# Kernel tuning notes

Hardware: AMD Instinct MI355X
Metric: run time of the kernel (lower is better)

Reference implementation:

```python
import jax, jax.numpy as jnp
import numpy as np

NUM_CLASSES = 4      # config.class_num (malaria stages)
N = 2048             # total nodes = source + target samples
S = 1024             # source_length
FEAT_IN = 25088      # VGG19 include_top=False -> 7*7*512 flattened
D_FC = 512           # Dense(512)
D_G1 = 512           # config.features_dim (GCNConv1 out)
D_G2 = 256           # config.GCN_hidderlayer_dim_num (GCNConv2 out)


def setup_inputs() -> dict:
    key = jax.random.key(0)
    ks = jax.random.split(key, 8)
    sc = lambda fan_in: np.float32(1.0 / np.sqrt(fan_in))
    return {
        "x": jax.random.normal(ks[0], (N, FEAT_IN), jnp.float32),
        "W_fc": jax.random.normal(ks[1], (FEAT_IN, D_FC), jnp.float32) * sc(FEAT_IN),
        "b_fc": jnp.zeros((D_FC,), jnp.float32),
        "W_g1": jax.random.normal(ks[2], (D_FC, D_G1), jnp.float32) * sc(D_FC),
        "b_g1": jnp.zeros((D_G1,), jnp.float32),
        "W_g2": jax.random.normal(ks[3], (D_G1, D_G2), jnp.float32) * sc(D_G1),
        "b_g2": jnp.zeros((D_G2,), jnp.float32),
        "source_labels": jax.random.randint(ks[4], (S,), 0, NUM_CLASSES),
        "source_length": S,
    }


def reference(x, W_fc, b_fc, W_g1, b_g1, W_g2, b_g2, source_labels, source_length):
    # fc after (omitted frozen) VGG19 backbone + flatten
    feats = x @ W_fc + b_fc                                   # [N, 512]

    # get_centers: per-class SUM of source features (no averaging, faithful)
    src = feats[:source_length]                               # [S, 512]
    centers = jax.ops.segment_sum(src, source_labels, num_segments=NUM_CLASSES)  # [C, 512]

    # per-target euclidean distance to each centroid + argmin
    # (argmin of squared distance == argmin of euclidean distance)
    tgt = feats[source_length:]                               # [T, 512]
    d2 = (jnp.sum(tgt * tgt, axis=1, keepdims=True)
          - 2.0 * (tgt @ centers.T)
          + jnp.sum(centers * centers, axis=1)[None, :])      # [T, C]
    target_labels = jnp.argmin(d2, axis=1)                    # [T] int

    # label-cluster graph: edge iff same label; source block forced to identity
    all_labels = jnp.concatenate([source_labels.astype(jnp.int32),
                                  target_labels.astype(jnp.int32)])
    adj = (all_labels[:, None] == all_labels[None, :]).astype(feats.dtype)  # [N, N]
    adj = adj.at[:source_length, :source_length].set(
        jnp.eye(source_length, dtype=feats.dtype))

    # add_self_loops(value=1) then symmetric gcn_filter D^-1/2 A D^-1/2
    A = adj + jnp.eye(N, dtype=feats.dtype)
    dinv = jax.lax.rsqrt(jnp.sum(A, axis=1))                  # [N]
    A_norm = dinv[:, None] * A * dinv[None, :]                # [N, N]

    # two GCN layers (spektral GCNConv: A_norm @ (X @ W) + b) with relu
    h = jax.nn.relu(A_norm @ (feats @ W_g1) + b_g1)           # [N, 512]
    h = jax.nn.relu(A_norm @ (h @ W_g2) + b_g2)               # [N, 256]
    return (h, A_norm, feats)
```

## Files before the change

### kernel.cpp

```cpp
#include <hip/hip_runtime.h>

#define NROWS 2048
#define SLEN  1024
#define FEAT  25088
#define DFC   512
#define DG1   512
#define DG2   256
#define CSPLIT 128

typedef __attribute__((ext_vector_type(8))) short short8;
typedef __attribute__((ext_vector_type(4))) float f32x4;

__device__ __forceinline__ unsigned short bfbits(float f) {
  unsigned int u = __float_as_uint(f);
  u += 0x7fffu + ((u >> 16) & 1u);
  return (unsigned short)(u >> 16);
}

__device__ __forceinline__ unsigned int cvtpk(float lo, float hi) {
  unsigned int r;
  asm("v_cvt_pk_bf16_f32 %0, %1, %2" : "=v"(r) : "v"(lo), "v"(hi));
  return r;
}

__device__ __forceinline__ void load_lds16(const void* g, void* l) {
  __builtin_amdgcn_global_load_lds(
      (const __attribute__((address_space(1))) unsigned int*)g,
      (__attribute__((address_space(3))) unsigned int*)l, 16, 0, 0);
}

__global__ void transpose_cvt_k(const float* __restrict__ src, unsigned short* __restrict__ dst,
                                int K, int Ncol) {
  __shared__ float tile[64][65];
  int kb = blockIdx.x * 64, nb = blockIdx.y * 64;
  int tx = threadIdx.x & 63, ty = threadIdx.x >> 6;
  #pragma unroll
  for (int i = ty; i < 64; i += 4)
    tile[i][tx] = src[(size_t)(kb + i) * Ncol + (nb + tx)];
  __syncthreads();
  #pragma unroll
  for (int i = ty; i < 64; i += 4)
    dst[(size_t)(nb + i) * K + (kb + tx)] = bfbits(tile[tx][i]);
}

__global__ __launch_bounds__(256, 4) void gemm_fc_k(const float* __restrict__ A,
    const unsigned short* __restrict__ BT, float* __restrict__ Cacc, int ksteps) {
  __shared__ unsigned short Al[128 * 32];
  __shared__ unsigned short Bl[128 * 32];
  const int K = FEAT;
  int tid = threadIdx.x;
  int m0 = (blockIdx.x >> 2) * 128;
  int n0 = (blockIdx.x & 3) * 128;
  int kbase = blockIdx.y * ksteps * 32;
  int wid = tid >> 6, lane = tid & 63;
  int wm = wid >> 1, wn = wid & 1;
  int lrow = lane & 15, lko = lane >> 4;

  int chA0 = tid, rA0 = chA0 >> 2, cA0 = chA0 & 3, pA0 = cA0 ^ ((rA0 >> 1) & 3);
  int chA1 = tid + 256, rA1 = chA1 >> 2, cA1 = chA1 & 3, pA1 = cA1 ^ ((rA1 >> 1) & 3);
  int chB0 = wid * 128 + lane;
  int chB1 = wid * 128 + 64 + lane;
  int rB0 = chB0 >> 2, cB0 = (chB0 & 3) ^ ((rB0 >> 1) & 3);
  int rB1 = chB1 >> 2, cB1 = (chB1 & 3) ^ ((rB1 >> 1) & 3);
  const float* gA0 = A + (size_t)(m0 + rA0) * K + cA0 * 8;
  const float* gA1 = A + (size_t)(m0 + rA1) * K + cA1 * 8;
  const unsigned short* gB0 = BT + (size_t)(n0 + rB0) * K + cB0 * 8;
  const unsigned short* gB1 = BT + (size_t)(n0 + rB1) * K + cB1 * 8;

  f32x4 acc[4][4];
  #pragma unroll
  for (int i = 0; i < 4; i++)
    #pragma unroll
    for (int j = 0; j < 4; j++) acc[i][j] = (f32x4){0.f, 0.f, 0.f, 0.f};

  for (int t = 0; t < ksteps; ++t) {
    int k0 = kbase + t * 32;
    float4 v00 = *reinterpret_cast<const float4*>(gA0 + k0);
    float4 v01 = *reinterpret_cast<const float4*>(gA0 + k0 + 4);
    float4 v10 = *reinterpret_cast<const float4*>(gA1 + k0);
    float4 v11 = *reinterpret_cast<const float4*>(gA1 + k0 + 4);
    int4 o0, o1;
    o0.x = (int)cvtpk(v00.x, v00.y); o0.y = (int)cvtpk(v00.z, v00.w);
    o0.z = (int)cvtpk(v01.x, v01.y); o0.w = (int)cvtpk(v01.z, v01.w);
    o1.x = (int)cvtpk(v10.x, v10.y); o1.y = (int)cvtpk(v10.z, v10.w);
    o1.z = (int)cvtpk(v11.x, v11.y); o1.w = (int)cvtpk(v11.z, v11.w);
    __syncthreads();
    *reinterpret_cast<int4*>((char*)Al + rA0 * 64 + pA0 * 16) = o0;
    *reinterpret_cast<int4*>((char*)Al + rA1 * 64 + pA1 * 16) = o1;
    load_lds16(gB0 + k0, (char*)Bl + chB0 * 16);
    load_lds16(gB1 + k0, (char*)Bl + chB1 * 16);
    __syncthreads();
    short8 af[4], bfv[4];
    #pragma unroll
    for (int mi = 0; mi < 4; mi++) {
      int R = wm * 64 + mi * 16 + lrow;
      int p = lko ^ ((R >> 1) & 3);
      af[mi] = *reinterpret_cast<const short8*>((char*)Al + R * 64 + p * 16);
    }
    #pragma unroll
    for (int ni = 0; ni < 4; ni++) {
      int R = wn * 64 + ni * 16 + lrow;
      int p = lko ^ ((R >> 1) & 3);
      bfv[ni] = *reinterpret_cast<const short8*>((char*)Bl + R * 64 + p * 16);
    }
    #pragma unroll
    for (int mi = 0; mi < 4; mi++)
      #pragma unroll
      for (int ni = 0; ni < 4; ni++)
        acc[mi][ni] = __builtin_amdgcn_mfma_f32_16x16x32_bf16(af[mi], bfv[ni], acc[mi][ni], 0, 0, 0);
  }

  #pragma unroll
  for (int mi = 0; mi < 4; mi++)
    #pragma unroll
    for (int ni = 0; ni < 4; ni++)
      #pragma unroll
      for (int r = 0; r < 4; r++) {
        int row = m0 + wm * 64 + mi * 16 + lko * 4 + r;
        int col = n0 + wn * 64 + ni * 16 + lrow;
        atomicAdd(&Cacc[(size_t)row * DFC + col], acc[mi][ni][r]);
      }
}

__global__ __launch_bounds__(256) void gemm_l_k(const unsigned short* __restrict__ A,
    const unsigned short* __restrict__ BT, float* __restrict__ Cacc,
    int K, int Ncols, int tiles_n, int ksteps) {
  __shared__ unsigned short Al[2][128 * 64];
  __shared__ unsigned short Bl[2][128 * 64];
  int tid = threadIdx.x;
  int m0 = (blockIdx.x / tiles_n) * 128;
  int n0 = (blockIdx.x % tiles_n) * 128;
  int kbase = blockIdx.y * ksteps * 64;
  int wid = tid >> 6, lane = tid & 63;
  int wm = wid >> 1, wn = wid & 1;
  int lrow = lane & 15, lko = lane >> 4;

  f32x4 acc[4][4];
  #pragma unroll
  for (int i = 0; i < 4; i++)
    #pragma unroll
    for (int j = 0; j < 4; j++) acc[i][j] = (f32x4){0.f, 0.f, 0.f, 0.f};

  auto stage = [&](unsigned short (*L)[128 * 64], const unsigned short* G, int buf, int k0) {
    #pragma unroll
    for (int j = 0; j < 4; j++) {
      int chb = j * 256 + wid * 64;
      int ch = chb + lane;
      int r = ch >> 3, c = (ch & 7) ^ (r & 7);
      load_lds16(G + (size_t)r * K + k0 + c * 8, (char*)L[buf] + chb * 16);
    }
  };

  stage(Al, A + (size_t)m0 * K, 0, kbase);
  stage(Bl, BT + (size_t)n0 * K, 0, kbase);
  __syncthreads();

  int cur = 0;
  for (int t = 0; t < ksteps; ++t) {
    bool more = (t + 1 < ksteps);
    if (more) {
      stage(Al, A + (size_t)m0 * K, cur ^ 1, kbase + (t + 1) * 64);
      stage(Bl, BT + (size_t)n0 * K, cur ^ 1, kbase + (t + 1) * 64);
    }
    #pragma unroll
    for (int kk = 0; kk < 2; kk++) {
      short8 af[4], bfv[4];
      #pragma unroll
      for (int mi = 0; mi < 4; mi++) {
        int R = wm * 64 + mi * 16 + lrow;
        int slot = ((kk << 2) | lko) ^ (lrow & 7);
        af[mi] = *reinterpret_cast<const short8*>((char*)Al[cur] + R * 128 + slot * 16);
      }
      #pragma unroll
      for (int ni = 0; ni < 4; ni++) {
        int R = wn * 64 + ni * 16 + lrow;
        int slot = ((kk << 2) | lko) ^ (lrow & 7);
        bfv[ni] = *reinterpret_cast<const short8*>((char*)Bl[cur] + R * 128 + slot * 16);
      }
      #pragma unroll
      for (int mi = 0; mi < 4; mi++)
        #pragma unroll
        for (int ni = 0; ni < 4; ni++)
          acc[mi][ni] = __builtin_amdgcn_mfma_f32_16x16x32_bf16(af[mi], bfv[ni], acc[mi][ni], 0, 0, 0);
    }
    __syncthreads();
    cur ^= 1;
  }
  #pragma unroll
  for (int mi = 0; mi < 4; mi++)
    #pragma unroll
    for (int ni = 0; ni < 4; ni++)
      #pragma unroll
      for (int r = 0; r < 4; r++) {
        int row = m0 + wm * 64 + mi * 16 + lko * 4 + r;
        int col = n0 + wn * 64 + ni * 16 + lrow;
        atomicAdd(&Cacc[(size_t)row * Ncols + col], acc[mi][ni][r]);
      }
}

__global__ void feats_fin_k(const float* __restrict__ facc, const float* __restrict__ bfc,
                            float* __restrict__ outf, unsigned short* __restrict__ outbf) {
  int i = blockIdx.y;
  int n = blockIdx.x * 256 + threadIdx.x;
  float v = facc[(size_t)i * DFC + n] + bfc[n];
  outf[(size_t)i * DFC + n] = v;
  outbf[(size_t)i * DFC + n] = bfbits(v);
}

__global__ void seg_sum_part_k(const float* __restrict__ x, const int* __restrict__ slab,
                               float* __restrict__ sxp) {
  int k4 = blockIdx.x * 256 + threadIdx.x;
  if (k4 >= FEAT / 4) return;
  int k = k4 * 4;
  int i0 = blockIdx.y * 64, i1 = i0 + 64;
  float4 a0 = {0,0,0,0}, a1 = {0,0,0,0}, a2 = {0,0,0,0}, a3 = {0,0,0,0};
  #pragma unroll 4
  for (int i = i0; i < i1; i++) {
    float4 v = *reinterpret_cast<const float4*>(x + (size_t)i * FEAT + k);
    int c = slab[i];
    float m0 = (c == 0) ? 1.f : 0.f, m1 = (c == 1) ? 1.f : 0.f;
    float m2 = (c == 2) ? 1.f : 0.f, m3 = (c == 3) ? 1.f : 0.f;
    a0.x += m0 * v.x; a0.y += m0 * v.y; a0.z += m0 * v.z; a0.w += m0 * v.w;
    a1.x += m1 * v.x; a1.y += m1 * v.y; a1.z += m1 * v.z; a1.w += m1 * v.w;
    a2.x += m2 * v.x; a2.y += m2 * v.y; a2.z += m2 * v.z; a2.w += m2 * v.w;
    a3.x += m3 * v.x; a3.y += m3 * v.y; a3.z += m3 * v.z; a3.w += m3 * v.w;
  }
  size_t base = (size_t)blockIdx.y * 4 * FEAT;
  *reinterpret_cast<float4*>(sxp + base + 0 * FEAT + k) = a0;
  *reinterpret_cast<float4*>(sxp + base + 1 * FEAT + k) = a1;
  *reinterpret_cast<float4*>(sxp + base + 2 * FEAT + k) = a2;
  *reinterpret_cast<float4*>(sxp + base + 3 * FEAT + k) = a3;
}

__global__ void seg_sum_reduce_k(const float* __restrict__ sxp, float* __restrict__ sx) {
  int k4 = blockIdx.x * 256 + threadIdx.x;
  if (k4 >= FEAT / 4) return;
  int k = k4 * 4;
  int c = blockIdx.y;
  double s0 = 0, s1 = 0, s2 = 0, s3 = 0;
  #pragma unroll
  for (int p = 0; p < 16; p++) {
    float4 v = *reinterpret_cast<const float4*>(sxp + ((size_t)p * 4 + c) * FEAT + k);
    s0 += (double)v.x; s1 += (double)v.y; s2 += (double)v.z; s3 += (double)v.w;
  }
  float4 r; r.x = (float)s0; r.y = (float)s1; r.z = (float)s2; r.w = (float)s3;
  *reinterpret_cast<float4*>(sx + (size_t)c * FEAT + k) = r;
}

__global__ void count_src_k(const int* __restrict__ slab, int* __restrict__ cnt) {
  __shared__ int c[4];
  if (threadIdx.x < 4) c[threadIdx.x] = 0;
  __syncthreads();
  for (int i = threadIdx.x; i < SLEN; i += 256) atomicAdd(&c[slab[i]], 1);
  __syncthreads();
  if (threadIdx.x < 4) cnt[threadIdx.x] = c[threadIdx.x];
}

__global__ void centers_part_k(const float* __restrict__ sx, const float* __restrict__ W,
                               double* __restrict__ cpart) {
  int n = blockIdx.x * 64 + (threadIdx.x & 63);
  int cc = threadIdx.x >> 6;
  int kb = blockIdx.y * (FEAT / CSPLIT), ke = kb + FEAT / CSPLIT;
  const float* sr = sx + (size_t)cc * FEAT;
  double acc = 0.0;
  #pragma unroll 4
  for (int k = kb; k < ke; k++)
    acc += (double)sr[k] * (double)W[(size_t)k * DFC + n];
  cpart[((size_t)blockIdx.y * 4 + cc) * DFC + n] = acc;
}

__global__ void centers_reduce_k(const double* __restrict__ cpart, const float* __restrict__ bfc,
                                 const int* __restrict__ cntsrc, float* __restrict__ Cent) {
  int idx = blockIdx.x * 256 + threadIdx.x;
  int cc = idx >> 9, n = idx & 511;
  double s = 0.0;
  #pragma unroll 4
  for (int p = 0; p < CSPLIT; p++) s += cpart[((size_t)p * 4 + cc) * DFC + n];
  Cent[idx] = (float)(s + (double)cntsrc[cc] * (double)bfc[n]);
}

__global__ void wc_k(const float* __restrict__ W, const float* __restrict__ Cent,
                     float* __restrict__ wc) {
  __shared__ float cs[4 * DFC];
  for (int i = threadIdx.x; i < 4 * DFC; i += 256) cs[i] = Cent[i];
  __syncthreads();
  int k = blockIdx.x * 256 + threadIdx.x;
  if (k >= FEAT) return;
  const float* wr = W + (size_t)k * DFC;
  double a0 = 0, a1 = 0, a2 = 0, a3 = 0;
  #pragma unroll 2
  for (int n = 0; n < DFC; n += 4) {
    float4 w4 = *reinterpret_cast<const float4*>(wr + n);
    a0 += (double)w4.x * cs[0 * DFC + n] + (double)w4.y * cs[0 * DFC + n + 1]
        + (double)w4.z * cs[0 * DFC + n + 2] + (double)w4.w * cs[0 * DFC + n + 3];
    a1 += (double)w4.x * cs[1 * DFC + n] + (double)w4.y * cs[1 * DFC + n + 1]
        + (double)w4.z * cs[1 * DFC + n + 2] + (double)w4.w * cs[1 * DFC + n + 3];
    a2 += (double)w4.x * cs[2 * DFC + n] + (double)w4.y * cs[2 * DFC + n + 1]
        + (double)w4.z * cs[2 * DFC + n + 2] + (double)w4.w * cs[2 * DFC + n + 3];
    a3 += (double)w4.x * cs[3 * DFC + n] + (double)w4.y * cs[3 * DFC + n + 1]
        + (double)w4.z * cs[3 * DFC + n + 2] + (double)w4.w * cs[3 * DFC + n + 3];
  }
  float4 r; r.x = (float)a0; r.y = (float)a1; r.z = (float)a2; r.w = (float)a3;
  *reinterpret_cast<float4*>(wc + 4 * (size_t)k) = r;
}

__global__ void kj_k(const float* __restrict__ Cent, const float* __restrict__ bfc,
                     float* __restrict__ Kj) {
  int j = threadIdx.x >> 6, lane = threadIdx.x & 63;
  float cn = 0.f, bc = 0.f;
  for (int n = lane; n < DFC; n += 64) {
    float c = Cent[j * DFC + n];
    cn += c * c; bc += bfc[n] * c;
  }
  #pragma unroll
  for (int m = 32; m >= 1; m >>= 1) { cn += __shfl_xor(cn, m); bc += __shfl_xor(bc, m); }
  if (lane == 0) Kj[j] = cn - 2.f * bc;
}

__global__ void d2_labels_k(const float* __restrict__ x, const float* __restrict__ wc,
                            const float* __restrict__ Kj, int* __restrict__ tlab) {
  int row = blockIdx.x;
  int tid = threadIdx.x;
  const float* xr = x + (size_t)(SLEN + row) * FEAT;
  double a0 = 0, a1 = 0, a2 = 0, a3 = 0;
  #pragma unroll 2
  for (int k = tid; k < FEAT; k += 256) {
    float xv = xr[k];
    float4 w4 = *reinterpret_cast<const float4*>(wc + 4 * (size_t)k);
    a0 += (double)xv * w4.x; a1 += (double)xv * w4.y;
    a2 += (double)xv * w4.z; a3 += (double)xv * w4.w;
  }
  #pragma unroll
  for (int m = 32; m >= 1; m >>= 1) {
    a0 += __shfl_xor(a0, m); a1 += __shfl_xor(a1, m);
    a2 += __shfl_xor(a2, m); a3 += __shfl_xor(a3, m);
  }
  __shared__ double s[4][4];
  int wid = tid >> 6, lane = tid & 63;
  if (lane == 0) { s[wid][0] = a0; s[wid][1] = a1; s[wid][2] = a2; s[wid][3] = a3; }
  __syncthreads();
  if (tid == 0) {
    double t0 = s[0][0] + s[1][0] + s[2][0] + s[3][0];
    double t1 = s[0][1] + s[1][1] + s[2][1] + s[3][1];
    double t2 = s[0][2] + s[1][2] + s[2][2] + s[3][2];
    double t3 = s[0][3] + s[1][3] + s[2][3] + s[3][3];
    double s0 = (double)Kj[0] - 2.0 * t0;
    double s1 = (double)Kj[1] - 2.0 * t1;
    double s2 = (double)Kj[2] - 2.0 * t2;
    double s3 = (double)Kj[3] - 2.0 * t3;
    int bi = 0; double b = s0;
    if (s1 < b) { b = s1; bi = 1; }
    if (s2 < b) { b = s2; bi = 2; }
    if (s3 < b) { b = s3; bi = 3; }
    tlab[row] = bi;
  }
}

__global__ void finalize_labels_k(const int* __restrict__ slab, const int* __restrict__ tlab,
                                  const int* __restrict__ cntsrc, int* __restrict__ alllab,
                                  float* __restrict__ dinv) {
  __shared__ int ct[4];
  if (threadIdx.x < 4) ct[threadIdx.x] = 0;
  __syncthreads();
  for (int i = threadIdx.x; i < SLEN; i += 256) atomicAdd(&ct[tlab[i]], 1);
  __syncthreads();
  for (int i = threadIdx.x; i < NROWS; i += 256) {
    int lab = (i < SLEN) ? slab[i] : tlab[i - SLEN];
    alllab[i] = lab;
    float rs = (i < SLEN) ? (2.f + (float)ct[lab])
                          : (1.f + (float)cntsrc[lab] + (float)ct[lab]);
    dinv[i] = 1.f / sqrtf(rs);
  }
}

__global__ void anorm_k(const int* __restrict__ alllab, const float* __restrict__ dinv,
                        float* __restrict__ Aout) {
  int i = blockIdx.y;
  int j0 = (blockIdx.x * 256 + threadIdx.x) * 4;
  int li = alllab[i];
  float di = dinv[i];
  int4 lj = *reinterpret_cast<const int4*>(alllab + j0);
  float4 dj = *reinterpret_cast<const float4*>(dinv + j0);
  int jj[4] = {lj.x, lj.y, lj.z, lj.w};
  float dd[4] = {dj.x, dj.y, dj.z, dj.w};
  float4 o;
  float* op = &o.x;
  #pragma unroll
  for (int e = 0; e < 4; e++) {
    int j = j0 + e;
    float v;
    if (i == j) v = 2.f * di * dd[e];
    else if (i < SLEN && j < SLEN) v = 0.f;
    else v = (li == jj[e]) ? di * dd[e] : 0.f;
    op[e] = v;
  }
  *reinterpret_cast<float4*>(Aout + (size_t)i * NROWS + j0) = o;
}

__global__ void reduce_st_k(const float* __restrict__ Xacc, const int* __restrict__ alllab,
                            const float* __restrict__ dinv, float* __restrict__ ST, int D) {
  int n = blockIdx.x * 256 + threadIdx.x;
  int i0 = blockIdx.y * 32, i1 = i0 + 32;
  float s[4] = {0, 0, 0, 0}, tt[4] = {0, 0, 0, 0};
  for (int i = i0; i < i1; ++i) {
    float v = dinv[i] * Xacc[(size_t)i * D + n];
    int lab = alllab[i];
    bool src = i < SLEN;
    #pragma unroll
    for (int c = 0; c < 4; c++) {
      s[c]  += (src && lab == c) ? v : 0.f;
      tt[c] += (!src && lab == c) ? v : 0.f;
    }
  }
  #pragma unroll
  for (int c = 0; c < 4; c++) {
    atomicAdd(&ST[c * D + n], s[c]);
    atomicAdd(&ST[(4 + c) * D + n], tt[c]);
  }
}

__global__ void apply_prop_k(const float* __restrict__ Xacc, const float* __restrict__ ST,
                             const int* __restrict__ alllab, const float* __restrict__ dinv,
                             const float* __restrict__ bias, float* __restrict__ outf,
                             unsigned short* __restrict__ outbf, int D) {
  int i = blockIdx.y;
  int n = blockIdx.x * 256 + threadIdx.x;
  float dv = dinv[i];
  int lab = alllab[i];
  float xv = Xacc[(size_t)i * D + n];
  float z;
  if (i < SLEN) z = dv * (2.f * dv * xv + ST[(4 + lab) * D + n]);
  else          z = dv * (ST[lab * D + n] + ST[(4 + lab) * D + n] + dv * xv);
  z += bias[n];
  z = fmaxf(z, 0.f);
  if (outf)  outf[(size_t)i * D + n] = z;
  if (outbf) outbf[(size_t)i * D + n] = bfbits(z);
}

extern "C" void kernel_launch(void* const* d_in, const int* in_sizes, int n_in,
                              void* d_out, int out_size, void* d_ws, size_t ws_size,
                              hipStream_t stream) {
  const float* x    = (const float*)d_in[0];
  const float* Wfc  = (const float*)d_in[1];
  const float* bfc  = (const float*)d_in[2];
  const float* Wg1  = (const float*)d_in[3];
  const float* bg1  = (const float*)d_in[4];
  const float* Wg2  = (const float*)d_in[5];
  const float* bg2  = (const float*)d_in[6];
  const int*   slab = (const int*)d_in[7];

  float* out = (float*)d_out;
  float* out_h = out;
  float* out_A = out + 524288;
  float* out_f = out + 4718592;

  char* w = (char*)d_ws;
  unsigned short* wT   = (unsigned short*)(w);
  unsigned short* g1T  = (unsigned short*)(w + 25690112);
  unsigned short* g2T  = (unsigned short*)(w + 26214400);
  float* facc          = (float*)(w + 26476544);
  unsigned short* fbf  = (unsigned short*)(w + 30670848);
  float* x1acc         = (float*)(w + 32768000);
  unsigned short* h1bf = (unsigned short*)(w + 36962304);
  float* x2acc         = (float*)(w + 39059456);
  float* sx            = (float*)(w + 41156608);
  float* Cent          = (float*)(w + 41623552);
  float* wc            = (float*)(w + 41631744);
  float* Kj            = (float*)(w + 42033152);
  int*   tlab          = (int*)(w + 42033216);
  int*   alllab        = (int*)(w + 42037312);
  float* dinv          = (float*)(w + 42045504);
  int*   cntsrc        = (int*)(w + 42053696);
  float* ST1           = (float*)(w + 42053760);
  float* ST2           = (float*)(w + 42070144);

  float*  sxp     = (float*)(w + 32768000);
  double* cpart_d = (double*)(w + 39059456);

  hipMemsetAsync(facc,  0, (size_t)NROWS * DFC * 4, stream);
  hipMemsetAsync(ST1,   0, 8 * DG1 * 4, stream);
  hipMemsetAsync(ST2,   0, 8 * DG2 * 4, stream);

  transpose_cvt_k<<<dim3(FEAT / 64, DFC / 64), 256, 0, stream>>>(Wfc, wT, FEAT, DFC);
  transpose_cvt_k<<<dim3(DFC / 64, DG1 / 64), 256, 0, stream>>>(Wg1, g1T, DFC, DG1);
  transpose_cvt_k<<<dim3(DG1 / 64, DG2 / 64), 256, 0, stream>>>(Wg2, g2T, DG1, DG2);

  gemm_fc_k<<<dim3(64, 16), 256, 0, stream>>>(x, wT, facc, 49);
  feats_fin_k<<<dim3(DFC / 256, NROWS), 256, 0, stream>>>(facc, bfc, out_f, fbf);

  seg_sum_part_k<<<dim3(25, 16), 256, 0, stream>>>(x, slab, sxp);
  seg_sum_reduce_k<<<dim3(25, 4), 256, 0, stream>>>(sxp, sx);
  count_src_k<<<1, 256, 0, stream>>>(slab, cntsrc);
  centers_part_k<<<dim3(DFC / 64, CSPLIT), 256, 0, stream>>>(sx, Wfc, cpart_d);
  centers_reduce_k<<<dim3(4 * DFC / 256), 256, 0, stream>>>(cpart_d, bfc, cntsrc, Cent);
  wc_k<<<dim3(FEAT / 256), 256, 0, stream>>>(Wfc, Cent, wc);
  kj_k<<<1, 256, 0, stream>>>(Cent, bfc, Kj);
  d2_labels_k<<<dim3(NROWS - SLEN), 256, 0, stream>>>(x, wc, Kj, tlab);
  finalize_labels_k<<<1, 256, 0, stream>>>(slab, tlab, cntsrc, alllab, dinv);

  anorm_k<<<dim3(NROWS / 1024, NROWS), 256, 0, stream>>>(alllab, dinv, out_A);

  hipMemsetAsync(x1acc, 0, (size_t)NROWS * DG1 * 4, stream);
  gemm_l_k<<<dim3(16 * 4, 4), 256, 0, stream>>>(fbf, g1T, x1acc, DFC, DG1, 4, 2);
  reduce_st_k<<<dim3(DG1 / 256, 64), 256, 0, stream>>>(x1acc, alllab, dinv, ST1, DG1);
  apply_prop_k<<<dim3(DG1 / 256, NROWS), 256, 0, stream>>>(x1acc, ST1, alllab, dinv, bg1,
                                                           nullptr, h1bf, DG1);

  hipMemsetAsync(x2acc, 0, (size_t)NROWS * DG2 * 4, stream);
  gemm_l_k<<<dim3(16 * 2, 8), 256, 0, stream>>>(h1bf, g2T, x2acc, DG1, DG2, 2, 1);
  reduce_st_k<<<dim3(DG2 / 256, 64), 256, 0, stream>>>(x2acc, alllab, dinv, ST2, DG2);
  apply_prop_k<<<dim3(DG2 / 256, NROWS), 256, 0, stream>>>(x2acc, ST2, alllab, dinv, bg2,
                                                           out_h, nullptr, DG2);

  (void)in_sizes; (void)n_in; (void)out_size; (void)ws_size;
}
```

Measured before the change: 393.6 us.

## Load FC GEMM fragments directly from global memory, bypassing LDS staging

The FC GEMM kernel no longer stages A and B tiles through shared memory with two barriers per k-step. Each lane now loads its MFMA fragments straight from global memory and converts A to bf16 in registers. Launch bounds drop to 3 blocks per CU to make room for the larger register footprint. This removes the LDS writes, reads and barriers, but each tile is now fetched redundantly by the waves that share it, which adds global/L2 traffic and uses smaller, less coalesced loads.

```diff
diff --git a/kernel.cpp b/kernel.cpp
--- a/kernel.cpp
+++ b/kernel.cpp
@@ -43,10 +43,8 @@
     dst[(size_t)(nb + i) * K + (kb + tx)] = bfbits(tile[tx][i]);
 }
 
-__global__ __launch_bounds__(256, 4) void gemm_fc_k(const float* __restrict__ A,
+__global__ __launch_bounds__(256, 3) void gemm_fc_k(const float* __restrict__ A,
     const unsigned short* __restrict__ BT, float* __restrict__ Cacc, int ksteps) {
-  __shared__ unsigned short Al[128 * 32];
-  __shared__ unsigned short Bl[128 * 32];
   const int K = FEAT;
   int tid = threadIdx.x;
   int m0 = (blockIdx.x >> 2) * 128;
@@ -56,16 +54,14 @@
   int wm = wid >> 1, wn = wid & 1;
   int lrow = lane & 15, lko = lane >> 4;
 
-  int chA0 = tid, rA0 = chA0 >> 2, cA0 = chA0 & 3, pA0 = cA0 ^ ((rA0 >> 1) & 3);
-  int chA1 = tid + 256, rA1 = chA1 >> 2, cA1 = chA1 & 3, pA1 = cA1 ^ ((rA1 >> 1) & 3);
-  int chB0 = wid * 128 + lane;
-  int chB1 = wid * 128 + 64 + lane;
-  int rB0 = chB0 >> 2, cB0 = (chB0 & 3) ^ ((rB0 >> 1) & 3);
-  int rB1 = chB1 >> 2, cB1 = (chB1 & 3) ^ ((rB1 >> 1) & 3);
-  const float* gA0 = A + (size_t)(m0 + rA0) * K + cA0 * 8;
-  const float* gA1 = A + (size_t)(m0 + rA1) * K + cA1 * 8;
-  const unsigned short* gB0 = BT + (size_t)(n0 + rB0) * K + cB0 * 8;
-  const unsigned short* gB1 = BT + (size_t)(n0 + rB1) * K + cB1 * 8;
+  const float* ap[4];
+  const unsigned short* bp[4];
+  #pragma unroll
+  for (int mi = 0; mi < 4; mi++)
+    ap[mi] = A + (size_t)(m0 + wm * 64 + mi * 16 + lrow) * K + kbase + lko * 8;
+  #pragma unroll
+  for (int ni = 0; ni < 4; ni++)
+    bp[ni] = BT + (size_t)(n0 + wn * 64 + ni * 16 + lrow) * K + kbase + lko * 8;
 
   f32x4 acc[4][4];
   #pragma unroll
@@ -74,34 +70,26 @@
     for (int j = 0; j < 4; j++) acc[i][j] = (f32x4){0.f, 0.f, 0.f, 0.f};
 
   for (int t = 0; t < ksteps; ++t) {
-    int k0 = kbase + t * 32;
-    float4 v00 = *reinterpret_cast<const float4*>(gA0 + k0);
-    float4 v01 = *reinterpret_cast<const float4*>(gA0 + k0 + 4);
-    float4 v10 = *reinterpret_cast<const float4*>(gA1 + k0);
-    float4 v11 = *reinterpret_cast<const float4*>(gA1 + k0 + 4);
-    int4 o0, o1;
-    o0.x = (int)cvtpk(v00.x, v00.y); o0.y = (int)cvtpk(v00.z, v00.w);
-    o0.z = (int)cvtpk(v01.x, v01.y); o0.w = (int)cvtpk(v01.z, v01.w);
-    o1.x = (int)cvtpk(v10.x, v10.y); o1.y = (int)cvtpk(v10.z, v10.w);
-    o1.z = (int)cvtpk(v11.x, v11.y); o1.w = (int)cvtpk(v11.z, v11.w);
-    __syncthreads();
-    *reinterpret_cast<int4*>((char*)Al + rA0 * 64 + pA0 * 16) = o0;
-    *reinterpret_cast<int4*>((char*)Al + rA1 * 64 + pA1 * 16) = o1;
-    load_lds16(gB0 + k0, (char*)Bl + chB0 * 16);
-    load_lds16(gB1 + k0, (char*)Bl + chB1 * 16);
-    __syncthreads();
-    short8 af[4], bfv[4];
+    int ko = t * 32;
+    float4 va[4][2];
+    short8 bfv[4];
     #pragma unroll
     for (int mi = 0; mi < 4; mi++) {
-      int R = wm * 64 + mi * 16 + lrow;
-      int p = lko ^ ((R >> 1) & 3);
-      af[mi] = *reinterpret_cast<const short8*>((char*)Al + R * 64 + p * 16);
+      va[mi][0] = *reinterpret_cast<const float4*>(ap[mi] + ko);
+      va[mi][1] = *reinterpret_cast<const float4*>(ap[mi] + ko + 4);
     }
     #pragma unroll
-    for (int ni = 0; ni < 4; ni++) {
-      int R = wn * 64 + ni * 16 + lrow;
-      int p = lko ^ ((R >> 1) & 3);
-      bfv[ni] = *reinterpret_cast<const short8*>((char*)Bl + R * 64 + p * 16);
+    for (int ni = 0; ni < 4; ni++)
+      bfv[ni] = *reinterpret_cast<const short8*>(bp[ni] + ko);
+    short8 af[4];
+    #pragma unroll
+    for (int mi = 0; mi < 4; mi++) {
+      int4 ai;
+      ai.x = (int)cvtpk(va[mi][0].x, va[mi][0].y);
+      ai.y = (int)cvtpk(va[mi][0].z, va[mi][0].w);
+      ai.z = (int)cvtpk(va[mi][1].x, va[mi][1].y);
+      ai.w = (int)cvtpk(va[mi][1].z, va[mi][1].w);
+      af[mi] = *reinterpret_cast<short8*>(&ai);
     }
     #pragma unroll
     for (int mi = 0; mi < 4; mi++)
```

Measured after the change: 544.6 us. 38.4% more time.
